# Optimization experiments

Hardware: AMD Instinct MI355X
Metric: run time of the kernel (lower is better)

## Reference

```python
import jax, jax.numpy as jnp
import numpy as np

B, S, D, H = 2, 2048, 1024, 16
DK = D // H


def setup_inputs() -> dict:
    key = jax.random.key(0)
    ks = jax.random.split(key, 11)
    s = 1.0 / np.sqrt(D)
    inp = {
        "q": jax.random.normal(ks[0], (B, S, D), jnp.float32),
        "k": jax.random.normal(ks[1], (B, S, D), jnp.float32),
        "v": jax.random.normal(ks[2], (B, S, D), jnp.float32),
        "mask": jnp.tril(jnp.ones((S, S), jnp.int32))[None, None],  # [1,1,S,S] causal
        "Wq": jax.random.normal(ks[3], (D, D), jnp.float32) * s,
        "bq": jnp.zeros((D,), jnp.float32),
        "Wk": jax.random.normal(ks[4], (D, D), jnp.float32) * s,
        "bk": jnp.zeros((D,), jnp.float32),
        "Wv": jax.random.normal(ks[5], (D, D), jnp.float32) * s,
        "bv": jnp.zeros((D,), jnp.float32),
        "Wo": jax.random.normal(ks[6], (D, D), jnp.float32) * s,
        "bo": jnp.zeros((D,), jnp.float32),
    }
    return inp


def reference(q, k, v, mask, Wq, bq, Wk, bk, Wv, bv, Wo, bo):
    # projections -> [B, H, S, DK]
    def split_heads(x):
        return x.reshape(B, S, H, DK).transpose(0, 2, 1, 3)

    Q = split_heads(q @ Wq + bq)
    K = split_heads(k @ Wk + bk)
    V = split_heads(v @ Wv + bv)

    scores = jnp.einsum("bhqd,bhkd->bhqk", Q, K) / jnp.sqrt(jnp.float32(DK))
    scores = jnp.where(mask == 0, jnp.float32(-1e9), scores)
    # source applies dropout(p=0.0) here -> identity
    attn = jax.nn.softmax(scores, axis=-1)  # [B,H,S,S]
    x = jnp.einsum("bhqk,bhkd->bhqd", attn, V)
    x = x.transpose(0, 2, 1, 3).reshape(B, S, D)
    return x @ Wo + bo
```

## Files before the change

kernel.cpp:

```cpp
#include <hip/hip_runtime.h>
#include <hip/hip_bf16.h>
#include <stdint.h>

#define Bb 2
#define Ss 2048
#define Dd 1024
#define Hh 16
#define DKk 64

#define QSCALE 0.180336878f

typedef __attribute__((ext_vector_type(8))) short s8v;
typedef __attribute__((ext_vector_type(4))) short s4v;
typedef __attribute__((ext_vector_type(4))) float f4v;
typedef __attribute__((ext_vector_type(16))) float f16v;

#if __has_builtin(__builtin_amdgcn_exp2f)
#define EXP2(x) __builtin_amdgcn_exp2f(x)
#else
#define EXP2(x) __expf((x)*0.69314718f)
#endif

__device__ __forceinline__ unsigned short f2bf(float f) {
    __hip_bfloat16 h = __float2bfloat16(f);
    union { __hip_bfloat16 h; unsigned short u; } c; c.h = h;
    return c.u;
}

__device__ __forceinline__ unsigned pack_bf2(float lo, float hi) {
    __hip_bfloat162 h = __float22bfloat162_rn(float2{lo, hi});
    union { __hip_bfloat162 h; unsigned u; } c; c.h = h;
    return c.u;
}

__device__ __forceinline__ void gload16(const void* g, void* l) {
    __builtin_amdgcn_global_load_lds((__attribute__((address_space(1))) void*)g,
                                     (__attribute__((address_space(3))) void*)l, 16, 0, 0);
}

__global__ void __launch_bounds__(256) prep_x(const float* __restrict__ q,
                                              const float* __restrict__ k,
                                              const float* __restrict__ v,
                                              unsigned short* __restrict__ xq,
                                              unsigned short* __restrict__ xk,
                                              unsigned short* __restrict__ xv) {
    const int z = blockIdx.z;
    const float* s = (z == 0) ? q : ((z == 1) ? k : v);
    unsigned short* d = (z == 0) ? xq : ((z == 1) ? xk : xv);
    long i = ((long)blockIdx.x * blockDim.x + threadIdx.x) * 8;
    f4v a = *(const f4v*)(s + i);
    f4v b = *(const f4v*)(s + i + 4);
    union { unsigned u[4]; s8v v; } o;
    o.u[0] = pack_bf2(a[0], a[1]);
    o.u[1] = pack_bf2(a[2], a[3]);
    o.u[2] = pack_bf2(b[0], b[1]);
    o.u[3] = pack_bf2(b[2], b[3]);
    *(s8v*)(void*)(d + i) = o.v;
}

__global__ void __launch_bounds__(256) prep_w(const float* __restrict__ Wq,
                                              const float* __restrict__ Wk,
                                              const float* __restrict__ Wv,
                                              const float* __restrict__ Wo,
                                              unsigned short* __restrict__ o0,
                                              unsigned short* __restrict__ o1,
                                              unsigned short* __restrict__ o2,
                                              unsigned short* __restrict__ o3) {
    __shared__ float t[64][65];
    const int z = blockIdx.z;
    const float* W = (z == 0) ? Wq : ((z == 1) ? Wk : ((z == 2) ? Wv : Wo));
    unsigned short* O = (z == 0) ? o0 : ((z == 1) ? o1 : ((z == 2) ? o2 : o3));
    const int n0 = (blockIdx.x & 15) * 64;
    const int k0 = (blockIdx.x >> 4) * 64;
    const int c = threadIdx.x & 63;
    const int r4 = threadIdx.x >> 6;
#pragma unroll
    for (int i = 0; i < 16; i++) {
        int r = i * 4 + r4;
        t[r][c] = W[(long)(k0 + r) * Dd + n0 + c];
    }
    __syncthreads();
#pragma unroll
    for (int i = 0; i < 16; i++) {
        int r = i * 4 + r4;
        O[(long)(n0 + r) * Dd + k0 + c] = f2bf(t[c][r]);
    }
}

template <int MODE>
__device__ __forceinline__ void gemm_body(const unsigned short* __restrict__ A,
                                          const unsigned short* __restrict__ Bt,
                                          const float* __restrict__ bias,
                                          void* __restrict__ out, float oscale,
                                          unsigned short* smem, int m0, int n0) {
    unsigned short* As = smem;
    unsigned short* Bs = smem + 128 * 64;
    const int tid = threadIdx.x;
    const int l = tid & 63;
    const int w = tid >> 6;
    const int wr = w >> 1, wc = w & 1;
    const int lr = l & 15, lg = l >> 4;

    f4v acc[4][4];
#pragma unroll
    for (int m = 0; m < 4; m++)
#pragma unroll
        for (int n = 0; n < 4; n++) acc[m][n] = (f4v){0.f, 0.f, 0.f, 0.f};

    const int srow = tid >> 3;
    const int sg = (tid & 7) ^ (srow & 7);
    char* lbaseA = (char*)As + w * 1024;
    char* lbaseB = (char*)Bs + w * 1024;

    for (int t = 0; t < 16; t++) {
        const int k0 = t * 64;
#pragma unroll
        for (int i = 0; i < 4; i++) {
            int rowA = i * 32 + srow;
            gload16((const char*)A + ((long)(m0 + rowA) * 1024 + k0) * 2 + sg * 16,
                    lbaseA + i * 4096);
            gload16((const char*)Bt + ((long)(n0 + rowA) * 1024 + k0) * 2 + sg * 16,
                    lbaseB + i * 4096);
        }
        __syncthreads();
#pragma unroll
        for (int kk = 0; kk < 2; kk++) {
            s8v af[4], bfr[4];
#pragma unroll
            for (int m = 0; m < 4; m++) {
                int row = wr * 64 + m * 16 + lr;
                int gc = (kk * 4 + lg) ^ (row & 7);
                af[m] = *(const s8v*)((const char*)As + row * 128 + gc * 16);
            }
#pragma unroll
            for (int n = 0; n < 4; n++) {
                int row = wc * 64 + n * 16 + lr;
                int gc = (kk * 4 + lg) ^ (row & 7);
                bfr[n] = *(const s8v*)((const char*)Bs + row * 128 + gc * 16);
            }
#pragma unroll
            for (int m = 0; m < 4; m++)
#pragma unroll
                for (int n = 0; n < 4; n++)
                    acc[m][n] = __builtin_amdgcn_mfma_f32_16x16x32_bf16(af[m], bfr[n],
                                                                        acc[m][n], 0, 0, 0);
        }
        __syncthreads();
    }

#pragma unroll
    for (int n = 0; n < 4; n++) {
        int col = n0 + wc * 64 + n * 16 + lr;
        float bv = bias[col];
#pragma unroll
        for (int m = 0; m < 4; m++) {
#pragma unroll
            for (int r = 0; r < 4; r++) {
                int row = m0 + wr * 64 + m * 16 + lg * 4 + r;
                float val = acc[m][n][r] + bv;
                if (MODE == 0) {
                    int b = row >> 11, s2 = row & 2047, h = col >> 6, d = col & 63;
                    ((unsigned short*)out)[(((b * Hh + h) * Ss + s2) << 6) + d] =
                        f2bf(val * oscale);
                } else if (MODE == 1) {
                    int b = row >> 11, s2 = row & 2047, h = col >> 6, d = col & 63;
                    ((unsigned short*)out)[((b * Hh + h) * DKk + d) * Ss + s2] = f2bf(val);
                } else {
                    ((float*)out)[(long)row * Dd + col] = val;
                }
            }
        }
    }
}

__device__ __forceinline__ void xcd_tile(int bid, int& m0, int& n0) {
    int content = (bid & 7) * 32 + (bid >> 3);
    n0 = (content & 7) * 128;
    m0 = (content >> 3) * 128;
}

__global__ void __launch_bounds__(256) qkv_gemm(const unsigned short* __restrict__ xq,
                                                const unsigned short* __restrict__ xk,
                                                const unsigned short* __restrict__ xv,
                                                const unsigned short* __restrict__ Wqt,
                                                const unsigned short* __restrict__ Wkt,
                                                const unsigned short* __restrict__ Wvt,
                                                const float* __restrict__ bq,
                                                const float* __restrict__ bk,
                                                const float* __restrict__ bv,
                                                unsigned short* __restrict__ Qh,
                                                unsigned short* __restrict__ Kh,
                                                unsigned short* __restrict__ Vt) {
    __shared__ unsigned short smem[128 * 64 * 2];
    int m0, n0;
    xcd_tile(blockIdx.x, m0, n0);
    const int z = blockIdx.z;
    if (z == 0)
        gemm_body<0>(xq, Wqt, bq, Qh, QSCALE, smem, m0, n0);
    else if (z == 1)
        gemm_body<0>(xk, Wkt, bk, Kh, 1.f, smem, m0, n0);
    else
        gemm_body<1>(xv, Wvt, bv, Vt, 1.f, smem, m0, n0);
}

__global__ void __launch_bounds__(256) out_gemm(const unsigned short* __restrict__ x,
                                                const unsigned short* __restrict__ Wot,
                                                const float* __restrict__ bo,
                                                float* __restrict__ out) {
    __shared__ unsigned short smem[128 * 64 * 2];
    int m0, n0;
    xcd_tile(blockIdx.x, m0, n0);
    gemm_body<2>(x, Wot, bo, out, 1.f, smem, m0, n0);
}

__global__ void __launch_bounds__(256) attn_kernel(const unsigned short* __restrict__ Qh,
                                                   const unsigned short* __restrict__ Kh,
                                                   const unsigned short* __restrict__ Vt,
                                                   unsigned short* __restrict__ xatt) {
    __shared__ __align__(16) char ldsbuf[32768];
    unsigned short* Ks = (unsigned short*)ldsbuf;
    unsigned short* Vs = (unsigned short*)(ldsbuf + 16384);
    const int tid = threadIdx.x;
    const int w = tid >> 6, l = tid & 63;
    const int lq = l & 31;
    const int hi = l >> 5;
    const int bh = blockIdx.x & 31;
    const int tile = 63 - (blockIdx.x >> 5);
    const int q0 = tile * 32;
    const int b = bh >> 4, h = bh & 15;
    const unsigned short* Qp = Qh + bh * Ss * DKk;
    const unsigned short* Kp = Kh + bh * Ss * DKk;
    const unsigned short* Vp = Vt + bh * DKk * Ss;

    s8v qf[4];
#pragma unroll
    for (int kk = 0; kk < 4; kk++)
        qf[kk] = *(const s8v*)(Qp + (q0 + lq) * 64 + kk * 16 + hi * 8);

    f16v oT0, oT1;
#pragma unroll
    for (int r = 0; r < 16; r++) { oT0[r] = 0.f; oT1[r] = 0.f; }
    float mx = -1e30f, sm = 0.f;
    const int nkb = tile + 1;
    const int nch = (nkb + 3) >> 2;

    for (int ch = 0; ch < nch; ch++) {
        const int kv0 = ch * 128;
#pragma unroll
        for (int i = 0; i < 4; i++) {
            const int G0 = i * 256 + w * 64;
            int G = G0 + l;
            int row = G >> 3, gd = G & 7;
            int gs = gd ^ (row & 7);
            gload16(Kp + (kv0 + row) * 64 + gs * 8, (char*)Ks + G0 * 16);
        }
#pragma unroll
        for (int i = 0; i < 4; i++) {
            const int G0 = i * 256 + w * 64;
            int G = G0 + l;
            int row = G >> 4, gd = G & 15;
            int gs = gd ^ (row & 15);
            gload16(Vp + (long)row * Ss + kv0 + gs * 8, (char*)Vs + G0 * 16);
        }
        __syncthreads();

        const int kb = ch * 4 + w;
        if (kb < nkb) {
            const int k0 = kb * 32;
            s8v kf[4];
#pragma unroll
            for (int kk = 0; kk < 4; kk++) {
                int row = w * 32 + lq;
                int g = (2 * kk + hi) ^ (row & 7);
                kf[kk] = *(const s8v*)((const char*)Ks + (row * 8 + g) * 16);
            }
            s8v vf0[2], vf1[2];
#pragma unroll
            for (int kk = 0; kk < 2; kk++) {
                int g0 = 4 * w + 2 * kk + hi;
                vf0[kk] = *(const s8v*)((const char*)Vs + (lq * 16 + (g0 ^ (lq & 15))) * 16);
                vf1[kk] =
                    *(const s8v*)((const char*)Vs + ((32 + lq) * 16 + (g0 ^ (lq & 15))) * 16);
            }

            f16v S;
#pragma unroll
            for (int r = 0; r < 16; r++) S[r] = 0.f;
#pragma unroll
            for (int kk = 0; kk < 4; kk++)
                S = __builtin_amdgcn_mfma_f32_32x32x16_bf16(kf[kk], qf[kk], S, 0, 0, 0);

            const bool diag = (kb == nkb - 1);
            float e[16];
#pragma unroll
            for (int r = 0; r < 16; r++) {
                float v = S[r];
                if (diag) {
                    int kv = k0 + (r & 3) + 8 * (r >> 2) + 4 * hi;
                    if (kv > q0 + lq) v = -1e30f;
                }
                e[r] = v;
            }
            float m8[8];
#pragma unroll
            for (int i = 0; i < 8; i++) m8[i] = fmaxf(e[i], e[i + 8]);
#pragma unroll
            for (int i = 0; i < 4; i++) m8[i] = fmaxf(m8[i], m8[i + 4]);
            float pmax = fmaxf(fmaxf(m8[0], m8[1]), fmaxf(m8[2], m8[3]));
            pmax = fmaxf(pmax, __shfl_xor(pmax, 32));

            if (!__all(pmax - mx <= 8.f)) {
                float mn = fmaxf(mx, pmax);
                float sc = EXP2(mx - mn);
                mx = mn;
                sm *= sc;
#pragma unroll
                for (int r = 0; r < 16; r++) { oT0[r] *= sc; oT1[r] *= sc; }
            }
#pragma unroll
            for (int r = 0; r < 16; r++) e[r] = EXP2(e[r] - mx);
            float s8s[8];
#pragma unroll
            for (int i = 0; i < 8; i++) s8s[i] = e[i] + e[i + 8];
#pragma unroll
            for (int i = 0; i < 4; i++) s8s[i] = s8s[i] + s8s[i + 4];
            float rs = (s8s[0] + s8s[1]) + (s8s[2] + s8s[3]);
            sm += rs + __shfl_xor(rs, 32);

            unsigned pk[8], sw[8];
#pragma unroll
            for (int i = 0; i < 8; i++) pk[i] = pack_bf2(e[2 * i], e[2 * i + 1]);
#pragma unroll
            for (int i = 0; i < 8; i++) sw[i] = (unsigned)__shfl_xor((int)pk[i], 32);
            union { unsigned u[4]; s8v v; } p0, p1;
            p0.u[0] = hi ? sw[2] : pk[0];
            p0.u[1] = hi ? sw[3] : pk[1];
            p0.u[2] = hi ? pk[2] : sw[0];
            p0.u[3] = hi ? pk[3] : sw[1];
            p1.u[0] = hi ? sw[6] : pk[4];
            p1.u[1] = hi ? sw[7] : pk[5];
            p1.u[2] = hi ? pk[6] : sw[4];
            p1.u[3] = hi ? pk[7] : sw[5];

            oT0 = __builtin_amdgcn_mfma_f32_32x32x16_bf16(vf0[0], p0.v, oT0, 0, 0, 0);
            oT0 = __builtin_amdgcn_mfma_f32_32x32x16_bf16(vf0[1], p1.v, oT0, 0, 0, 0);
            oT1 = __builtin_amdgcn_mfma_f32_32x32x16_bf16(vf1[0], p0.v, oT1, 0, 0, 0);
            oT1 = __builtin_amdgcn_mfma_f32_32x32x16_bf16(vf1[1], p1.v, oT1, 0, 0, 0);
        }
        __syncthreads();
    }

    float(*plds)[64][34] = (float(*)[64][34])ldsbuf;
    if (w >= 2) {
        float* p = plds[w - 2][l];
        p[0] = mx; p[1] = sm;
#pragma unroll
        for (int r = 0; r < 16; r++) { p[2 + r] = oT0[r]; p[18 + r] = oT1[r]; }
    }
    __syncthreads();
    if (w < 2) {
        const float* p = plds[w][l];
        float m2 = p[0], s2 = p[1];
        float M = fmaxf(mx, m2);
        float a = EXP2(mx - M), bb = EXP2(m2 - M);
        sm = sm * a + s2 * bb;
#pragma unroll
        for (int r = 0; r < 16; r++) {
            oT0[r] = oT0[r] * a + p[2 + r] * bb;
            oT1[r] = oT1[r] * a + p[18 + r] * bb;
        }
        mx = M;
    }
    __syncthreads();
    if (w == 1) {
        float* p = plds[0][l];
        p[0] = mx; p[1] = sm;
#pragma unroll
        for (int r = 0; r < 16; r++) { p[2 + r] = oT0[r]; p[18 + r] = oT1[r]; }
    }
    __syncthreads();
    if (w != 0) return;
    {
        const float* p = plds[0][l];
        float m2 = p[0], s2 = p[1];
        float M = fmaxf(mx, m2);
        float a = EXP2(mx - M), bb = EXP2(m2 - M);
        sm = sm * a + s2 * bb;
#pragma unroll
        for (int r = 0; r < 16; r++) {
            oT0[r] = oT0[r] * a + p[2 + r] * bb;
            oT1[r] = oT1[r] * a + p[18 + r] * bb;
        }
    }

    const float inv = 1.f / sm;
    const int q = q0 + lq;
    unsigned short* orow = xatt + (long)(b * Ss + q) * Dd + h * 64;
#pragma unroll
    for (int g = 0; g < 4; g++) {
        union { unsigned u[2]; s4v v; } v0, v1;
        v0.u[0] = pack_bf2(oT0[g * 4 + 0] * inv, oT0[g * 4 + 1] * inv);
        v0.u[1] = pack_bf2(oT0[g * 4 + 2] * inv, oT0[g * 4 + 3] * inv);
        v1.u[0] = pack_bf2(oT1[g * 4 + 0] * inv, oT1[g * 4 + 1] * inv);
        v1.u[1] = pack_bf2(oT1[g * 4 + 2] * inv, oT1[g * 4 + 3] * inv);
        int d = 8 * g + 4 * hi;
        *(s4v*)(orow + d) = v0.v;
        *(s4v*)(orow + 32 + d) = v1.v;
    }
}

extern "C" void kernel_launch(void* const* d_in, const int* in_sizes, int n_in,
                              void* d_out, int out_size, void* d_ws, size_t ws_size,
                              hipStream_t stream) {
    const float* q  = (const float*)d_in[0];
    const float* k  = (const float*)d_in[1];
    const float* v  = (const float*)d_in[2];
    const float* Wq = (const float*)d_in[4];
    const float* bq = (const float*)d_in[5];
    const float* Wk = (const float*)d_in[6];
    const float* bk = (const float*)d_in[7];
    const float* Wv = (const float*)d_in[8];
    const float* bv = (const float*)d_in[9];
    const float* Wo = (const float*)d_in[10];
    const float* bo = (const float*)d_in[11];
    float* out = (float*)d_out;

    char* ws = (char*)d_ws;
    unsigned short* xq  = (unsigned short*)(ws + 0);
    unsigned short* xk  = (unsigned short*)(ws + 8388608);
    unsigned short* xv  = (unsigned short*)(ws + 16777216);
    unsigned short* Wqt = (unsigned short*)(ws + 25165824);
    unsigned short* Wkt = (unsigned short*)(ws + 27262976);
    unsigned short* Wvt = (unsigned short*)(ws + 29360128);
    unsigned short* Wot = (unsigned short*)(ws + 31457280);
    unsigned short* Qh  = (unsigned short*)(ws + 33554432);
    unsigned short* Kh  = (unsigned short*)(ws + 41943040);
    unsigned short* Vtp = (unsigned short*)(ws + 50331648);
    unsigned short* xat = (unsigned short*)(ws + 58720256);

    prep_x<<<dim3(2048, 1, 3), 256, 0, stream>>>(q, k, v, xq, xk, xv);
    prep_w<<<dim3(256, 1, 4), 256, 0, stream>>>(Wq, Wk, Wv, Wo, Wqt, Wkt, Wvt, Wot);
    qkv_gemm<<<dim3(256, 1, 3), 256, 0, stream>>>(xq, xk, xv, Wqt, Wkt, Wvt,
                                                  bq, bk, bv, Qh, Kh, Vtp);
    attn_kernel<<<dim3(2048), 256, 0, stream>>>(Qh, Kh, Vtp, xat);
    out_gemm<<<dim3(256), 256, 0, stream>>>(xat, Wot, bo, out);
}
```

Before: 143.2 us.

## Overlap next K-tile global-to-LDS loads with MFMA in projection GEMM

Restructures the projection GEMM main loop to load all LDS fragments for a K-tile into registers first, barrier, then issue the global-to-LDS loads for the next tile before running the MFMAs. This is meant to hide global memory latency behind matrix compute using a single LDS buffer with register double-buffering. It raises register pressure (16 s8v fragments held at once) and relies on explicit waitcnt and barrier placement for correctness.

```diff
diff --git a/kernel.cpp b/kernel.cpp
--- a/kernel.cpp
+++ b/kernel.cpp
@@ -112,41 +112,57 @@
     char* lbaseA = (char*)As + w * 1024;
     char* lbaseB = (char*)Bs + w * 1024;
 
+#define STAGE_T(t_)                                                                    \
+    do {                                                                               \
+        const int k0_ = (t_) * 64;                                                     \
+        _Pragma("unroll") for (int i_ = 0; i_ < 4; i_++) {                             \
+            int rowA_ = i_ * 32 + srow;                                                \
+            gload16((const char*)A + ((long)(m0 + rowA_) * 1024 + k0_) * 2 + sg * 16,  \
+                    lbaseA + i_ * 4096);                                               \
+            gload16((const char*)Bt + ((long)(n0 + rowA_) * 1024 + k0_) * 2 + sg * 16, \
+                    lbaseB + i_ * 4096);                                               \
+        }                                                                              \
+    } while (0)
+
+    STAGE_T(0);
     for (int t = 0; t < 16; t++) {
-        const int k0 = t * 64;
-#pragma unroll
-        for (int i = 0; i < 4; i++) {
-            int rowA = i * 32 + srow;
-            gload16((const char*)A + ((long)(m0 + rowA) * 1024 + k0) * 2 + sg * 16,
-                    lbaseA + i * 4096);
-            gload16((const char*)Bt + ((long)(n0 + rowA) * 1024 + k0) * 2 + sg * 16,
-                    lbaseB + i * 4096);
-        }
-        __syncthreads();
+        asm volatile("s_waitcnt vmcnt(0)" ::: "memory");
+        __builtin_amdgcn_s_barrier();
+        __builtin_amdgcn_sched_barrier(0);
+
+        s8v af[2][4], bfr[2][4];
 #pragma unroll
         for (int kk = 0; kk < 2; kk++) {
-            s8v af[4], bfr[4];
 #pragma unroll
             for (int m = 0; m < 4; m++) {
                 int row = wr * 64 + m * 16 + lr;
                 int gc = (kk * 4 + lg) ^ (row & 7);
-                af[m] = *(const s8v*)((const char*)As + row * 128 + gc * 16);
+                af[kk][m] = *(const s8v*)((const char*)As + row * 128 + gc * 16);
             }
 #pragma unroll
             for (int n = 0; n < 4; n++) {
                 int row = wc * 64 + n * 16 + lr;
                 int gc = (kk * 4 + lg) ^ (row & 7);
-                bfr[n] = *(const s8v*)((const char*)Bs + row * 128 + gc * 16);
-            }
+                bfr[kk][n] = *(const s8v*)((const char*)Bs + row * 128 + gc * 16);
+            }
+        }
+        asm volatile("s_waitcnt lgkmcnt(0)" ::: "memory");
+        __builtin_amdgcn_sched_barrier(0);
+        __builtin_amdgcn_s_barrier();
+        __builtin_amdgcn_sched_barrier(0);
+
+        if (t + 1 < 16) STAGE_T(t + 1);
+
+#pragma unroll
+        for (int kk = 0; kk < 2; kk++)
 #pragma unroll
             for (int m = 0; m < 4; m++)
 #pragma unroll
                 for (int n = 0; n < 4; n++)
-                    acc[m][n] = __builtin_amdgcn_mfma_f32_16x16x32_bf16(af[m], bfr[n],
-                                                                        acc[m][n], 0, 0, 0);
-        }
-        __syncthreads();
-    }
+                    acc[m][n] = __builtin_amdgcn_mfma_f32_16x16x32_bf16(
+                        af[kk][m], bfr[kk][n], acc[m][n], 0, 0, 0);
+    }
+#undef STAGE_T
 
 #pragma unroll
     for (int n = 0; n < 4; n++) {
```

Measured after the change: 134.3 us. 1.07x faster.
